# Kernel tuning notes

Hardware: AMD Instinct MI355X
Metric: run time of the kernel (lower is better)

Reference implementation:

```python
import jax, jax.numpy as jnp
import numpy as np

D_MODEL = 1024
N_HEADS = 16
B, T = 16, 512


def setup_inputs() -> dict:
    key = jax.random.key(0)
    ks = jax.random.split(key, 5)
    s = 0.02
    return {
        "x": jax.random.normal(ks[0], (B, T, D_MODEL), dtype=jnp.float32),
        "w_qkv": jax.random.normal(ks[1], (D_MODEL, 3 * D_MODEL), dtype=jnp.float32) * s,
        "b_qkv": jax.random.normal(ks[2], (3 * D_MODEL,), dtype=jnp.float32) * s,
        "w_o": jax.random.normal(ks[3], (D_MODEL, D_MODEL), dtype=jnp.float32) * s,
        "b_o": jax.random.normal(ks[4], (D_MODEL,), dtype=jnp.float32) * s,
    }


def reference(x, w_qkv, b_qkv, w_o, b_o):
    Bx, Tx, C = x.shape
    H = N_HEADS
    hd = C // H
    qkv = x @ w_qkv + b_qkv                      # [B,T,3C]
    qkv = qkv.reshape(Bx, Tx, 3, H, hd).transpose(2, 0, 3, 1, 4)  # [3,B,H,T,hd]
    q, k, v = qkv[0], qkv[1], qkv[2]
    # NOTE: original scales by sqrt(C) = sqrt(d_model), not sqrt(head_dim)
    att = jnp.einsum("bhqd,bhkd->bhqk", q, k) / jnp.sqrt(jnp.float32(C))
    causal = jnp.tril(jnp.ones((Tx, Tx), dtype=bool))
    att = jnp.where(causal, att, -jnp.inf)
    att = jax.nn.softmax(att, axis=-1)
    y = jnp.einsum("bhqk,bhkd->bhqd", att, v)    # [B,H,T,hd]
    y = y.transpose(0, 2, 1, 3).reshape(Bx, Tx, C)
    return y @ w_o + b_o
```

## Files before the change

### kernel.cpp

```cpp
#include <hip/hip_runtime.h>
#include <cstddef>


#define B_  16
#define T_  512
#define C_  1024
#define H_  16
#define HD_ 64

typedef __bf16 bf16x8 __attribute__((ext_vector_type(8)));
typedef float  f32x4  __attribute__((ext_vector_type(4)));

__device__ __forceinline__ void gload16(const void* g, void* lds_dst) {
  __builtin_amdgcn_global_load_lds(
      (const __attribute__((address_space(1))) unsigned int*)g,
      (__attribute__((address_space(3))) unsigned int*)lds_dst, 16, 0, 0);
}

__global__ void cvt_kernel(const float* __restrict__ in, __bf16* __restrict__ out, int n) {
  int i = (blockIdx.x * 256 + threadIdx.x) * 8;
  if (i >= n) return;
  float4 f0 = *(const float4*)&in[i];
  float4 f1 = *(const float4*)&in[i + 4];
  bf16x8 o;
  o[0] = (__bf16)f0.x; o[1] = (__bf16)f0.y; o[2] = (__bf16)f0.z; o[3] = (__bf16)f0.w;
  o[4] = (__bf16)f1.x; o[5] = (__bf16)f1.y; o[6] = (__bf16)f1.z; o[7] = (__bf16)f1.w;
  *(bf16x8*)&out[i] = o;
}

__global__ void tconv_kernel(const float* __restrict__ w, __bf16* __restrict__ wt,
                             int K, int N) {
  __shared__ float tile[32][33];
  int tx = threadIdx.x, ty = threadIdx.y;
  int n0 = blockIdx.x * 32, k0 = blockIdx.y * 32;
  #pragma unroll
  for (int i = 0; i < 4; ++i) {
    int r = ty + i * 8;
    tile[r][tx] = w[(size_t)(k0 + r) * N + n0 + tx];
  }
  __syncthreads();
  #pragma unroll
  for (int i = 0; i < 4; ++i) {
    int r = ty + i * 8;
    wt[(size_t)(n0 + r) * K + k0 + tx] = (__bf16)tile[tx][r];
  }
}

__global__ __launch_bounds__(256) void gemmsq_kernel(
    const __bf16* __restrict__ A, const __bf16* __restrict__ BT,
    const float* __restrict__ bias, int K, int NBn,
    __bf16* __restrict__ oq, __bf16* __restrict__ okk, __bf16* __restrict__ ovt)
{
  __shared__ __attribute__((aligned(16))) char lds[32768];
  const int tid = threadIdx.x, lane = tid & 63, wid = tid >> 6;
  const int wm = wid >> 1, wn = wid & 1;
  const int lr = lane & 15, lg = lane >> 4;

  const int cpx = gridDim.x >> 3;
  const int id = (blockIdx.x & 7) * cpx + (blockIdx.x >> 3);
  const int m0 = (id / NBn) * 128, n0 = (id % NBn) * 128;

  const int r8  = wid * 8 + (lane >> 3);
  const int csw = ((lane & 7) ^ (lane >> 3)) * 8;

  auto stage = [&](const __bf16* g, char* dst) {
    #pragma unroll
    for (int i = 0; i < 4; ++i)
      gload16(g + (size_t)(i * 32 + r8) * K + csw, dst + i * 4096 + wid * 1024);
  };
  auto rd = [&](bf16x8* d, const char* buf, int woff) {
    #pragma unroll
    for (int f = 0; f < 4; ++f) {
      const char* rp = buf + (woff + f * 16 + lr) * 128;
      #pragma unroll
      for (int ks = 0; ks < 2; ++ks)
        d[f * 2 + ks] = *(const bf16x8*)(rp + (((ks << 2) + lg) ^ (lr & 7)) * 16);
    }
  };

  f32x4 acc[4][4] = {};
  const int nt = K >> 6;
  const __bf16* gA = A  + (size_t)m0 * K;
  const __bf16* gB = BT + (size_t)n0 * K;
  char* const Ab = lds;
  char* const Bb = lds + 16384;

  stage(gA, Ab);
  stage(gB, Bb);
  asm volatile("s_waitcnt vmcnt(0)\ns_barrier" ::: "memory");

  bf16x8 a[8], b[8];
  for (int t = 0; t < nt; ++t) {
    rd(a, Ab, wm * 64);
    rd(b, Bb, wn * 64);
    asm volatile("s_waitcnt lgkmcnt(0)\ns_barrier" ::: "memory");
    if (t + 1 < nt) {
      stage(gA + (size_t)(t + 1) * 64, Ab);
      stage(gB + (size_t)(t + 1) * 64, Bb);
    }
    __builtin_amdgcn_s_setprio(1);
    #pragma unroll
    for (int mf = 0; mf < 4; ++mf)
      #pragma unroll
      for (int nf = 0; nf < 4; ++nf)
        #pragma unroll
        for (int ks = 0; ks < 2; ++ks)
          acc[mf][nf] = __builtin_amdgcn_mfma_f32_16x16x32_bf16(
              a[mf * 2 + ks], b[nf * 2 + ks], acc[mf][nf], 0, 0, 0);
    __builtin_amdgcn_s_setprio(0);
    asm volatile("s_waitcnt vmcnt(0)\ns_barrier" ::: "memory");
  }

  #pragma unroll
  for (int nf = 0; nf < 4; ++nf) {
    int n = n0 + wn * 64 + nf * 16 + lr;
    float bv = bias[n];
    int which = n >> 10;
    int h = (n >> 6) & 15, d = n & 63;
    if (which == 2) {
      #pragma unroll
      for (int mf = 0; mf < 4; ++mf) {
        int m = m0 + wm * 64 + mf * 16 + lg * 4;
        int bb = m >> 9, t0 = m & 511;
        ushort4 pk;
        __bf16 e0 = (__bf16)(acc[mf][nf][0] + bv);
        __bf16 e1 = (__bf16)(acc[mf][nf][1] + bv);
        __bf16 e2 = (__bf16)(acc[mf][nf][2] + bv);
        __bf16 e3 = (__bf16)(acc[mf][nf][3] + bv);
        pk.x = *(unsigned short*)&e0; pk.y = *(unsigned short*)&e1;
        pk.z = *(unsigned short*)&e2; pk.w = *(unsigned short*)&e3;
        *(ushort4*)&ovt[(size_t)((bb * H_ + h) * HD_ + d) * T_ + t0] = pk;
      }
    } else {
      __bf16* dst = (which == 0) ? oq : okk;
      #pragma unroll
      for (int mf = 0; mf < 4; ++mf)
        #pragma unroll
        for (int j = 0; j < 4; ++j) {
          int m = m0 + wm * 64 + mf * 16 + lg * 4 + j;
          int bb = m >> 9, tt = m & 511;
          dst[(size_t)((bb * H_ + h) * T_ + tt) * HD_ + d] =
              (__bf16)(acc[mf][nf][j] + bv);
        }
    }
  }
}

__global__ __launch_bounds__(256) void gemmsq_o_kernel(
    const __bf16* __restrict__ A, const __bf16* __restrict__ BT,
    const float* __restrict__ bias, int K, int NBn, int N,
    float* __restrict__ out32)
{
  __shared__ __attribute__((aligned(16))) char lds[32768];
  const int tid = threadIdx.x, lane = tid & 63, wid = tid >> 6;
  const int wm = wid >> 1, wn = wid & 1;
  const int lr = lane & 15, lg = lane >> 4;

  const int cpx = gridDim.x >> 3;
  const int id = (blockIdx.x & 7) * cpx + (blockIdx.x >> 3);
  const int m0 = (id / NBn) * 128, n0 = (id % NBn) * 128;

  const int r8  = wid * 8 + (lane >> 3);
  const int csw = ((lane & 7) ^ (lane >> 3)) * 8;

  auto stage = [&](const __bf16* g, char* dst) {
    #pragma unroll
    for (int i = 0; i < 4; ++i)
      gload16(g + (size_t)(i * 32 + r8) * K + csw, dst + i * 4096 + wid * 1024);
  };
  auto rd = [&](bf16x8* d, const char* buf, int woff) {
    #pragma unroll
    for (int f = 0; f < 4; ++f) {
      const char* rp = buf + (woff + f * 16 + lr) * 128;
      #pragma unroll
      for (int ks = 0; ks < 2; ++ks)
        d[f * 2 + ks] = *(const bf16x8*)(rp + (((ks << 2) + lg) ^ (lr & 7)) * 16);
    }
  };

  f32x4 acc[4][4] = {};
  const int nt = K >> 6;
  const __bf16* gA = A  + (size_t)m0 * K;
  const __bf16* gB = BT + (size_t)n0 * K;
  char* const Ab = lds;
  char* const Bb = lds + 16384;

  stage(gA, Ab);
  stage(gB, Bb);
  asm volatile("s_waitcnt vmcnt(0)\ns_barrier" ::: "memory");

  bf16x8 a[8], b[8];
  for (int t = 0; t < nt; ++t) {
    rd(a, Ab, wm * 64);
    rd(b, Bb, wn * 64);
    asm volatile("s_waitcnt lgkmcnt(0)\ns_barrier" ::: "memory");
    if (t + 1 < nt) {
      stage(gA + (size_t)(t + 1) * 64, Ab);
      stage(gB + (size_t)(t + 1) * 64, Bb);
    }
    __builtin_amdgcn_s_setprio(1);
    #pragma unroll
    for (int mf = 0; mf < 4; ++mf)
      #pragma unroll
      for (int nf = 0; nf < 4; ++nf)
        #pragma unroll
        for (int ks = 0; ks < 2; ++ks)
          acc[mf][nf] = __builtin_amdgcn_mfma_f32_16x16x32_bf16(
              a[mf * 2 + ks], b[nf * 2 + ks], acc[mf][nf], 0, 0, 0);
    __builtin_amdgcn_s_setprio(0);
    asm volatile("s_waitcnt vmcnt(0)\ns_barrier" ::: "memory");
  }

  #pragma unroll
  for (int nf = 0; nf < 4; ++nf) {
    int n = n0 + wn * 64 + nf * 16 + lr;
    float bv = bias[n];
    #pragma unroll
    for (int mf = 0; mf < 4; ++mf)
      #pragma unroll
      for (int j = 0; j < 4; ++j) {
        int m = m0 + wm * 64 + mf * 16 + lg * 4 + j;
        out32[(size_t)m * N + n] = acc[mf][nf][j] + bv;
      }
  }
}

__global__ __launch_bounds__(256, 2) void attn_kernel(
    const __bf16* __restrict__ qb, const __bf16* __restrict__ kb,
    const __bf16* __restrict__ vtb, __bf16* __restrict__ y)
{
  __shared__ __attribute__((aligned(16))) __bf16 Ks[64][72];
  __shared__ __attribute__((aligned(16))) __bf16 Vt[64][72];
  __shared__ __attribute__((aligned(16))) __bf16 Ps[4][16][72];

  const int tid = threadIdx.x, lane = tid & 63, w = tid >> 6;
  const int lr = lane & 15, lg = lane >> 4;
  const int bh = blockIdx.x, qt = blockIdx.y;
  const size_t base = (size_t)bh * T_ * HD_;
  const int q0 = qt * 64 + w * 16;
  const float SCALE = 0.03125f;
  const float L2E = 1.44269504088896f;

  const int r_  = tid >> 3;
  const int c8_ = (tid & 7) * 8;

  bf16x8 qf[2];
  #pragma unroll
  for (int s = 0; s < 2; ++s)
    qf[s] = *(const bf16x8*)&qb[base + (size_t)(q0 + lr) * HD_ + s * 32 + lg * 8];

  f32x4 acc[4] = {};
  float mrun[4] = { -__builtin_inff(), -__builtin_inff(),
                    -__builtin_inff(), -__builtin_inff() };
  float lrun[4] = { 0.f, 0.f, 0.f, 0.f };

  bf16x8 kk[2], vv[2], kk2[2], vv2[2];
  #pragma unroll
  for (int p = 0; p < 2; ++p) {
    int rr = p * 32 + r_;
    kk[p] = *(const bf16x8*)&kb[base + (size_t)rr * HD_ + c8_];
    vv[p] = *(const bf16x8*)&vtb[base + (size_t)rr * T_ + c8_];
  }

  for (int c = 0; c <= qt; ++c) {
    #pragma unroll
    for (int p = 0; p < 2; ++p) {
      int rr = p * 32 + r_;
      *(bf16x8*)&Ks[rr][c8_] = kk[p];
      *(bf16x8*)&Vt[rr][c8_] = vv[p];
    }
    __syncthreads();

    if (c < qt) {
      #pragma unroll
      for (int p = 0; p < 2; ++p) {
        int rr = p * 32 + r_;
        kk2[p] = *(const bf16x8*)&kb[base + (size_t)(c + 1) * 64 * HD_ + (size_t)rr * HD_ + c8_];
        vv2[p] = *(const bf16x8*)&vtb[base + (size_t)rr * T_ + (c + 1) * 64 + c8_];
      }
    }

    f32x4 sc[4] = {};
    #pragma unroll
    for (int s = 0; s < 2; ++s) {
      #pragma unroll
      for (int cc = 0; cc < 4; ++cc) {
        bf16x8 kf = *(const bf16x8*)&Ks[cc * 16 + lr][s * 32 + lg * 8];
        sc[cc] = __builtin_amdgcn_mfma_f32_16x16x32_bf16(qf[s], kf, sc[cc], 0, 0, 0);
      }
    }

    #pragma unroll
    for (int cc = 0; cc < 4; ++cc)
      #pragma unroll
      for (int j = 0; j < 4; ++j) {
        float v = sc[cc][j] * SCALE;
        if (c == qt) {
          int kv = c * 64 + cc * 16 + lr;
          int qr = q0 + lg * 4 + j;
          if (kv > qr) v = -__builtin_inff();
        }
        sc[cc][j] = v;
      }

    float mx[4];
    #pragma unroll
    for (int j = 0; j < 4; ++j)
      mx[j] = fmaxf(fmaxf(sc[0][j], sc[1][j]), fmaxf(sc[2][j], sc[3][j]));
    #pragma unroll
    for (int msk = 1; msk <= 8; msk <<= 1)
      #pragma unroll
      for (int j = 0; j < 4; ++j)
        mx[j] = fmaxf(mx[j], __shfl_xor(mx[j], msk, 64));
    float corr[4];
    #pragma unroll
    for (int j = 0; j < 4; ++j) {
      float nm = fmaxf(mrun[j], mx[j]);
      corr[j] = exp2f((mrun[j] - nm) * L2E);
      mrun[j] = nm;
    }
    #pragma unroll
    for (int cc = 0; cc < 4; ++cc)
      #pragma unroll
      for (int j = 0; j < 4; ++j)
        sc[cc][j] = exp2f((sc[cc][j] - mrun[j]) * L2E);
    float rs[4];
    #pragma unroll
    for (int j = 0; j < 4; ++j)
      rs[j] = sc[0][j] + sc[1][j] + sc[2][j] + sc[3][j];
    #pragma unroll
    for (int msk = 1; msk <= 8; msk <<= 1)
      #pragma unroll
      for (int j = 0; j < 4; ++j)
        rs[j] += __shfl_xor(rs[j], msk, 64);
    #pragma unroll
    for (int j = 0; j < 4; ++j)
      lrun[j] = lrun[j] * corr[j] + rs[j];
    #pragma unroll
    for (int dd = 0; dd < 4; ++dd)
      #pragma unroll
      for (int j = 0; j < 4; ++j)
        acc[dd][j] *= corr[j];

    #pragma unroll
    for (int cc = 0; cc < 4; ++cc)
      #pragma unroll
      for (int j = 0; j < 4; ++j)
        Ps[w][lg * 4 + j][cc * 16 + lr] = (__bf16)sc[cc][j];

    #pragma unroll
    for (int s = 0; s < 2; ++s) {
      bf16x8 pa = *(const bf16x8*)&Ps[w][lr][s * 32 + lg * 8];
      #pragma unroll
      for (int dd = 0; dd < 4; ++dd) {
        bf16x8 vf = *(const bf16x8*)&Vt[dd * 16 + lr][s * 32 + lg * 8];
        acc[dd] = __builtin_amdgcn_mfma_f32_16x16x32_bf16(pa, vf, acc[dd], 0, 0, 0);
      }
    }
    __syncthreads();
    #pragma unroll
    for (int p = 0; p < 2; ++p) { kk[p] = kk2[p]; vv[p] = vv2[p]; }
  }

  const int b = bh >> 4, h = bh & 15;
  #pragma unroll
  for (int dd = 0; dd < 4; ++dd)
    #pragma unroll
    for (int j = 0; j < 4; ++j) {
      int t = q0 + lg * 4 + j;
      int d = dd * 16 + lr;
      y[((size_t)(b * T_ + t)) * C_ + h * HD_ + d] = (__bf16)(acc[dd][j] / lrun[j]);
    }
}

extern "C" void kernel_launch(void* const* d_in, const int* in_sizes, int n_in,
                              void* d_out, int out_size, void* d_ws, size_t ws_size,
                              hipStream_t stream) {
  const float* x    = (const float*)d_in[0];
  const float* wqkv = (const float*)d_in[1];
  const float* bqkv = (const float*)d_in[2];
  const float* wo   = (const float*)d_in[3];
  const float* bo   = (const float*)d_in[4];
  float* out = (float*)d_out;

  char* ws = (char*)d_ws;
  const size_t MB = 1u << 20;
  __bf16* xb    = (__bf16*)(ws);
  __bf16* wqt   = (__bf16*)(ws + 16 * MB);
  __bf16* wot   = (__bf16*)(ws + 22 * MB);
  __bf16* qbuf  = (__bf16*)(ws + 24 * MB);
  __bf16* kbuf  = (__bf16*)(ws + 40 * MB);
  __bf16* vtbuf = (__bf16*)(ws + 56 * MB);
  __bf16* ybuf  = (__bf16*)(ws + 72 * MB);

  const int NX = B_ * T_ * C_;
  cvt_kernel<<<NX / (256 * 8), 256, 0, stream>>>(x, xb, NX);
  tconv_kernel<<<dim3(3 * C_ / 32, C_ / 32), dim3(32, 8), 0, stream>>>(wqkv, wqt, C_, 3 * C_);
  tconv_kernel<<<dim3(C_ / 32, C_ / 32), dim3(32, 8), 0, stream>>>(wo, wot, C_, C_);

  gemmsq_kernel<<<1536, 256, 0, stream>>>(
      xb, wqt, bqkv, C_, 24, qbuf, kbuf, vtbuf);

  attn_kernel<<<dim3(B_ * H_, T_ / 64), 256, 0, stream>>>(qbuf, kbuf, vtbuf, ybuf);

  gemmsq_o_kernel<<<512, 256, 0, stream>>>(
      ybuf, wot, bo, C_, 8, C_, out);
}
```

Baseline: 139.8 us.

## Restructure attention to 32x32 MFMA with transposed scores and register-resident P

Rewrites the attention kernel so each block covers 128 queries with one 32-query tile per wave, computing S^T with 32x32x16 bf16 MFMA so each lane owns a single query row. The P tile is packed to bf16 and exchanged across lane halves with shuffles instead of going through LDS, which removes the Ps buffer and most cross-lane reductions. K/V LDS tiles are double-buffered, so the trailing barrier is dropped, and waves skip key chunks past their causal limit. Outputs are written as packed 4-element stores. The cost is half as many blocks, more registers per thread, and uneven per-wave work inside a block.

```diff
diff --git a/kernel.cpp b/kernel.cpp
--- a/kernel.cpp
+++ b/kernel.cpp
@@ -10,11 +10,19 @@
 
 typedef __bf16 bf16x8 __attribute__((ext_vector_type(8)));
 typedef float  f32x4  __attribute__((ext_vector_type(4)));
+typedef float  f32x16 __attribute__((ext_vector_type(16)));
 
 __device__ __forceinline__ void gload16(const void* g, void* lds_dst) {
   __builtin_amdgcn_global_load_lds(
       (const __attribute__((address_space(1))) unsigned int*)g,
       (__attribute__((address_space(3))) unsigned int*)lds_dst, 16, 0, 0);
+}
+
+__device__ __forceinline__ unsigned pack2(float a, float b) {
+  __bf16 x = (__bf16)a, y = (__bf16)b;
+  unsigned short ux = __builtin_bit_cast(unsigned short, x);
+  unsigned short uy = __builtin_bit_cast(unsigned short, y);
+  return (unsigned)ux | ((unsigned)uy << 16);
 }
 
 __global__ void cvt_kernel(const float* __restrict__ in, __bf16* __restrict__ out, int n) {
@@ -225,34 +233,34 @@
   }
 }
 
-__global__ __launch_bounds__(256, 2) void attn_kernel(
+__global__ __launch_bounds__(256) void attn_kernel(
     const __bf16* __restrict__ qb, const __bf16* __restrict__ kb,
     const __bf16* __restrict__ vtb, __bf16* __restrict__ y)
 {
-  __shared__ __attribute__((aligned(16))) __bf16 Ks[64][72];
-  __shared__ __attribute__((aligned(16))) __bf16 Vt[64][72];
-  __shared__ __attribute__((aligned(16))) __bf16 Ps[4][16][72];
+  __shared__ __attribute__((aligned(16))) __bf16 Ks[2][64][72];
+  __shared__ __attribute__((aligned(16))) __bf16 Vt[2][64][72];
 
   const int tid = threadIdx.x, lane = tid & 63, w = tid >> 6;
-  const int lr = lane & 15, lg = lane >> 4;
+  const int ql = lane & 31, hi = lane >> 5;
   const int bh = blockIdx.x, qt = blockIdx.y;
   const size_t base = (size_t)bh * T_ * HD_;
-  const int q0 = qt * 64 + w * 16;
+  const int b = bh >> 4, h = bh & 15;
+  const int q0w = qt * 128 + w * 32;
+  const int cl_w = q0w >> 6;
+  const int nc = 2 * qt + 2;
   const float SCALE = 0.03125f;
   const float L2E = 1.44269504088896f;
 
   const int r_  = tid >> 3;
   const int c8_ = (tid & 7) * 8;
 
-  bf16x8 qf[2];
-  #pragma unroll
-  for (int s = 0; s < 2; ++s)
-    qf[s] = *(const bf16x8*)&qb[base + (size_t)(q0 + lr) * HD_ + s * 32 + lg * 8];
-
-  f32x4 acc[4] = {};
-  float mrun[4] = { -__builtin_inff(), -__builtin_inff(),
-                    -__builtin_inff(), -__builtin_inff() };
-  float lrun[4] = { 0.f, 0.f, 0.f, 0.f };
+  bf16x8 qf[4];
+  #pragma unroll
+  for (int s = 0; s < 4; ++s)
+    qf[s] = *(const bf16x8*)&qb[base + (size_t)(q0w + ql) * HD_ + s * 16 + hi * 8];
+
+  f32x16 acc[2] = {};
+  float mrun = -__builtin_inff(), lrun = 0.f;
 
   bf16x8 kk[2], vv[2], kk2[2], vv2[2];
   #pragma unroll
@@ -262,114 +270,120 @@
     vv[p] = *(const bf16x8*)&vtb[base + (size_t)rr * T_ + c8_];
   }
 
-  for (int c = 0; c <= qt; ++c) {
+  for (int c = 0; c < nc; ++c) {
+    const int cb = c & 1;
     #pragma unroll
     for (int p = 0; p < 2; ++p) {
       int rr = p * 32 + r_;
-      *(bf16x8*)&Ks[rr][c8_] = kk[p];
-      *(bf16x8*)&Vt[rr][c8_] = vv[p];
+      *(bf16x8*)&Ks[cb][rr][c8_] = kk[p];
+      *(bf16x8*)&Vt[cb][rr][c8_] = vv[p];
     }
     __syncthreads();
 
-    if (c < qt) {
+    if (c + 1 < nc) {
       #pragma unroll
       for (int p = 0; p < 2; ++p) {
         int rr = p * 32 + r_;
-        kk2[p] = *(const bf16x8*)&kb[base + (size_t)(c + 1) * 64 * HD_ + (size_t)rr * HD_ + c8_];
+        kk2[p] = *(const bf16x8*)&kb[base + (size_t)((c + 1) * 64 + rr) * HD_ + c8_];
         vv2[p] = *(const bf16x8*)&vtb[base + (size_t)rr * T_ + (c + 1) * 64 + c8_];
       }
     }
 
-    f32x4 sc[4] = {};
-    #pragma unroll
-    for (int s = 0; s < 2; ++s) {
-      #pragma unroll
-      for (int cc = 0; cc < 4; ++cc) {
-        bf16x8 kf = *(const bf16x8*)&Ks[cc * 16 + lr][s * 32 + lg * 8];
-        sc[cc] = __builtin_amdgcn_mfma_f32_16x16x32_bf16(qf[s], kf, sc[cc], 0, 0, 0);
+    if (c <= cl_w) {
+      f32x16 sc[2] = {};
+      #pragma unroll
+      for (int ka = 0; ka < 2; ++ka)
+        #pragma unroll
+        for (int s = 0; s < 4; ++s) {
+          bf16x8 kf = *(const bf16x8*)&Ks[cb][ka * 32 + ql][s * 16 + hi * 8];
+          sc[ka] = __builtin_amdgcn_mfma_f32_32x32x16_bf16(kf, qf[s], sc[ka], 0, 0, 0);
+        }
+
+      const int qg = q0w + ql;
+      #pragma unroll
+      for (int ka = 0; ka < 2; ++ka)
+        #pragma unroll
+        for (int r = 0; r < 16; ++r) {
+          float v = sc[ka][r] * SCALE;
+          if (c == cl_w) {
+            int kvg = c * 64 + ka * 32 + (r & 3) + 8 * (r >> 2) + 4 * hi;
+            if (kvg > qg) v = -__builtin_inff();
+          }
+          sc[ka][r] = v;
+        }
+
+      float mx = sc[0][0];
+      #pragma unroll
+      for (int ka = 0; ka < 2; ++ka)
+        #pragma unroll
+        for (int r = 0; r < 16; ++r) mx = fmaxf(mx, sc[ka][r]);
+      mx = fmaxf(mx, __shfl_xor(mx, 32, 64));
+      float nm = fmaxf(mrun, mx);
+      float corr = exp2f((mrun - nm) * L2E);
+      mrun = nm;
+
+      float rs = 0.f;
+      #pragma unroll
+      for (int ka = 0; ka < 2; ++ka)
+        #pragma unroll
+        for (int r = 0; r < 16; ++r) {
+          float p = exp2f((sc[ka][r] - nm) * L2E);
+          sc[ka][r] = p;
+          rs += p;
+        }
+      rs += __shfl_xor(rs, 32, 64);
+      lrun = lrun * corr + rs;
+      #pragma unroll
+      for (int da = 0; da < 2; ++da)
+        #pragma unroll
+        for (int r = 0; r < 16; ++r) acc[da][r] *= corr;
+
+      unsigned pk[2][4][2];
+      #pragma unroll
+      for (int ka = 0; ka < 2; ++ka)
+        #pragma unroll
+        for (int m4 = 0; m4 < 4; ++m4)
+          #pragma unroll
+          for (int jh = 0; jh < 2; ++jh)
+            pk[ka][m4][jh] = pack2(sc[ka][4 * m4 + 2 * jh], sc[ka][4 * m4 + 2 * jh + 1]);
+
+      #pragma unroll
+      for (int sp = 0; sp < 4; ++sp) {
+        const int bb2 = sp & 1, kap = sp >> 1;
+        const int mo = 2 * bb2 + hi;
+        const int mp = 2 * bb2 + (hi ^ 1);
+        unsigned own0 = pk[kap][mo][0], own1 = pk[kap][mo][1];
+        unsigned rcv0 = (unsigned)__shfl_xor((int)pk[kap][mp][0], 32, 64);
+        unsigned rcv1 = (unsigned)__shfl_xor((int)pk[kap][mp][1], 32, 64);
+        uint4 wds;
+        if (hi == 0) { wds.x = own0; wds.y = own1; wds.z = rcv0; wds.w = rcv1; }
+        else         { wds.x = rcv0; wds.y = rcv1; wds.z = own0; wds.w = own1; }
+        bf16x8 pb = __builtin_bit_cast(bf16x8, wds);
+        #pragma unroll
+        for (int da = 0; da < 2; ++da) {
+          bf16x8 vf = *(const bf16x8*)&Vt[cb][da * 32 + ql][sp * 16 + hi * 8];
+          acc[da] = __builtin_amdgcn_mfma_f32_32x32x16_bf16(vf, pb, acc[da], 0, 0, 0);
+        }
       }
     }
 
     #pragma unroll
-    for (int cc = 0; cc < 4; ++cc)
-      #pragma unroll
-      for (int j = 0; j < 4; ++j) {
-        float v = sc[cc][j] * SCALE;
-        if (c == qt) {
-          int kv = c * 64 + cc * 16 + lr;
-          int qr = q0 + lg * 4 + j;
-          if (kv > qr) v = -__builtin_inff();
-        }
-        sc[cc][j] = v;
-      }
-
-    float mx[4];
-    #pragma unroll
-    for (int j = 0; j < 4; ++j)
-      mx[j] = fmaxf(fmaxf(sc[0][j], sc[1][j]), fmaxf(sc[2][j], sc[3][j]));
-    #pragma unroll
-    for (int msk = 1; msk <= 8; msk <<= 1)
-      #pragma unroll
-      for (int j = 0; j < 4; ++j)
-        mx[j] = fmaxf(mx[j], __shfl_xor(mx[j], msk, 64));
-    float corr[4];
-    #pragma unroll
-    for (int j = 0; j < 4; ++j) {
-      float nm = fmaxf(mrun[j], mx[j]);
-      corr[j] = exp2f((mrun[j] - nm) * L2E);
-      mrun[j] = nm;
-    }
-    #pragma unroll
-    for (int cc = 0; cc < 4; ++cc)
-      #pragma unroll
-      for (int j = 0; j < 4; ++j)
-        sc[cc][j] = exp2f((sc[cc][j] - mrun[j]) * L2E);
-    float rs[4];
-    #pragma unroll
-    for (int j = 0; j < 4; ++j)
-      rs[j] = sc[0][j] + sc[1][j] + sc[2][j] + sc[3][j];
-    #pragma unroll
-    for (int msk = 1; msk <= 8; msk <<= 1)
-      #pragma unroll
-      for (int j = 0; j < 4; ++j)
-        rs[j] += __shfl_xor(rs[j], msk, 64);
-    #pragma unroll
-    for (int j = 0; j < 4; ++j)
-      lrun[j] = lrun[j] * corr[j] + rs[j];
-    #pragma unroll
-    for (int dd = 0; dd < 4; ++dd)
-      #pragma unroll
-      for (int j = 0; j < 4; ++j)
-        acc[dd][j] *= corr[j];
-
-    #pragma unroll
-    for (int cc = 0; cc < 4; ++cc)
-      #pragma unroll
-      for (int j = 0; j < 4; ++j)
-        Ps[w][lg * 4 + j][cc * 16 + lr] = (__bf16)sc[cc][j];
-
-    #pragma unroll
-    for (int s = 0; s < 2; ++s) {
-      bf16x8 pa = *(const bf16x8*)&Ps[w][lr][s * 32 + lg * 8];
-      #pragma unroll
-      for (int dd = 0; dd < 4; ++dd) {
-        bf16x8 vf = *(const bf16x8*)&Vt[dd * 16 + lr][s * 32 + lg * 8];
-        acc[dd] = __builtin_amdgcn_mfma_f32_16x16x32_bf16(pa, vf, acc[dd], 0, 0, 0);
-      }
-    }
-    __syncthreads();
-    #pragma unroll
     for (int p = 0; p < 2; ++p) { kk[p] = kk2[p]; vv[p] = vv2[p]; }
   }
 
-  const int b = bh >> 4, h = bh & 15;
-  #pragma unroll
-  for (int dd = 0; dd < 4; ++dd)
-    #pragma unroll
-    for (int j = 0; j < 4; ++j) {
-      int t = q0 + lg * 4 + j;
-      int d = dd * 16 + lr;
-      y[((size_t)(b * T_ + t)) * C_ + h * HD_ + d] = (__bf16)(acc[dd][j] / lrun[j]);
+  float inv = 1.f / lrun;
+  #pragma unroll
+  for (int da = 0; da < 2; ++da)
+    #pragma unroll
+    for (int m4 = 0; m4 < 4; ++m4) {
+      ushort4 pkv;
+      __bf16 e0 = (__bf16)(acc[da][4 * m4 + 0] * inv);
+      __bf16 e1 = (__bf16)(acc[da][4 * m4 + 1] * inv);
+      __bf16 e2 = (__bf16)(acc[da][4 * m4 + 2] * inv);
+      __bf16 e3 = (__bf16)(acc[da][4 * m4 + 3] * inv);
+      pkv.x = *(unsigned short*)&e0; pkv.y = *(unsigned short*)&e1;
+      pkv.z = *(unsigned short*)&e2; pkv.w = *(unsigned short*)&e3;
+      *(ushort4*)&y[(size_t)(b * T_ + q0w + ql) * C_ + h * HD_ + da * 32 + m4 * 8 + hi * 4] = pkv;
     }
 }
 
@@ -401,7 +415,7 @@
   gemmsq_kernel<<<1536, 256, 0, stream>>>(
       xb, wqt, bqkv, C_, 24, qbuf, kbuf, vtbuf);
 
-  attn_kernel<<<dim3(B_ * H_, T_ / 64), 256, 0, stream>>>(qbuf, kbuf, vtbuf, ybuf);
+  attn_kernel<<<dim3(B_ * H_, 4), 256, 0, stream>>>(qbuf, kbuf, vtbuf, ybuf);
 
   gemmsq_o_kernel<<<512, 256, 0, stream>>>(
       ybuf, wot, bo, C_, 8, C_, out);
```

New measurement: 152.6 us. 9.2% more time.

## Load full per-head K/V into LDS once and loop query groups per block

Applied to the files above, without the earlier changes.

The attention kernel now launches one 512-thread block per (batch, head). Each block loads the whole K and transposed V for that head into about 146 KB of dynamic LDS through direct global-to-LDS loads with an XOR swizzle, then each wave processes four 16-row query groups. This removes the repeated K/V reloads and the per-tile barriers of the old 64-query-tile grid. The trade-off is fewer blocks (256), one block per CU because of the large LDS footprint, and causal work that is unevenly balanced across waves.

```diff
diff --git a/kernel.cpp b/kernel.cpp
--- a/kernel.cpp
+++ b/kernel.cpp
@@ -225,152 +225,147 @@
   }
 }
 
-__global__ __launch_bounds__(256, 2) void attn_kernel(
+__global__ __launch_bounds__(512) void attn_kernel(
     const __bf16* __restrict__ qb, const __bf16* __restrict__ kb,
     const __bf16* __restrict__ vtb, __bf16* __restrict__ y)
 {
-  __shared__ __attribute__((aligned(16))) __bf16 Ks[64][72];
-  __shared__ __attribute__((aligned(16))) __bf16 Vt[64][72];
-  __shared__ __attribute__((aligned(16))) __bf16 Ps[4][16][72];
+  extern __shared__ __align__(16) char smem[];
+  char* const Ksb = smem;
+  char* const Vtb = smem + 65536;
+  __bf16* const Ps = (__bf16*)(smem + 131072);
 
   const int tid = threadIdx.x, lane = tid & 63, w = tid >> 6;
   const int lr = lane & 15, lg = lane >> 4;
-  const int bh = blockIdx.x, qt = blockIdx.y;
+  const int bh = blockIdx.x;
   const size_t base = (size_t)bh * T_ * HD_;
-  const int q0 = qt * 64 + w * 16;
+  const int b = bh >> 4, h = bh & 15;
   const float SCALE = 0.03125f;
   const float L2E = 1.44269504088896f;
 
-  const int r_  = tid >> 3;
-  const int c8_ = (tid & 7) * 8;
-
-  bf16x8 qf[2];
-  #pragma unroll
-  for (int s = 0; s < 2; ++s)
-    qf[s] = *(const bf16x8*)&qb[base + (size_t)(q0 + lr) * HD_ + s * 32 + lg * 8];
-
-  f32x4 acc[4] = {};
-  float mrun[4] = { -__builtin_inff(), -__builtin_inff(),
-                    -__builtin_inff(), -__builtin_inff() };
-  float lrun[4] = { 0.f, 0.f, 0.f, 0.f };
-
-  bf16x8 kk[2], vv[2], kk2[2], vv2[2];
-  #pragma unroll
-  for (int p = 0; p < 2; ++p) {
-    int rr = p * 32 + r_;
-    kk[p] = *(const bf16x8*)&kb[base + (size_t)rr * HD_ + c8_];
-    vv[p] = *(const bf16x8*)&vtb[base + (size_t)rr * T_ + c8_];
-  }
-
-  for (int c = 0; c <= qt; ++c) {
-    #pragma unroll
-    for (int p = 0; p < 2; ++p) {
-      int rr = p * 32 + r_;
-      *(bf16x8*)&Ks[rr][c8_] = kk[p];
-      *(bf16x8*)&Vt[rr][c8_] = vv[p];
-    }
-    __syncthreads();
-
-    if (c < qt) {
-      #pragma unroll
-      for (int p = 0; p < 2; ++p) {
-        int rr = p * 32 + r_;
-        kk2[p] = *(const bf16x8*)&kb[base + (size_t)(c + 1) * 64 * HD_ + (size_t)rr * HD_ + c8_];
-        vv2[p] = *(const bf16x8*)&vtb[base + (size_t)rr * T_ + (c + 1) * 64 + c8_];
-      }
-    }
-
-    f32x4 sc[4] = {};
-    #pragma unroll
-    for (int s = 0; s < 2; ++s) {
-      #pragma unroll
-      for (int cc = 0; cc < 4; ++cc) {
-        bf16x8 kf = *(const bf16x8*)&Ks[cc * 16 + lr][s * 32 + lg * 8];
-        sc[cc] = __builtin_amdgcn_mfma_f32_16x16x32_bf16(qf[s], kf, sc[cc], 0, 0, 0);
-      }
-    }
-
-    #pragma unroll
-    for (int cc = 0; cc < 4; ++cc)
+  {
+    const int rk = tid >> 3;
+    const int sk = (tid & 7) ^ (rk & 7);
+    const int rv = tid >> 6;
+    const int sv = (tid & 63) ^ rv;
+    #pragma unroll
+    for (int i = 0; i < 8; ++i) {
+      gload16(kb  + base + (size_t)(i * 64 + rk) * HD_ + sk * 8,
+              Ksb + i * 8192 + w * 1024);
+      gload16(vtb + base + (size_t)(i * 8 + rv) * T_ + sv * 8,
+              Vtb + i * 8192 + w * 1024);
+    }
+  }
+  asm volatile("s_waitcnt vmcnt(0)\ns_barrier" ::: "memory");
+
+  #pragma unroll 1
+  for (int k = 0; k < 4; ++k) {
+    const int G = w + 8 * k;
+    const int q0 = G * 16;
+    const int cG = G >> 2;
+
+    bf16x8 qf[2];
+    #pragma unroll
+    for (int s = 0; s < 2; ++s)
+      qf[s] = *(const bf16x8*)&qb[base + (size_t)(q0 + lr) * HD_ + s * 32 + lg * 8];
+
+    f32x4 acc[4] = {};
+    float mrun[4] = { -__builtin_inff(), -__builtin_inff(),
+                      -__builtin_inff(), -__builtin_inff() };
+    float lrun[4] = { 0.f, 0.f, 0.f, 0.f };
+
+    for (int c = 0; c <= cG; ++c) {
+      f32x4 sc[4] = {};
+      #pragma unroll
+      for (int s = 0; s < 2; ++s) {
+        #pragma unroll
+        for (int cc = 0; cc < 4; ++cc) {
+          const char* kp = Ksb + (size_t)(c * 64 + cc * 16 + lr) * 128
+                               + (((s << 2) + lg) ^ (lr & 7)) * 16;
+          bf16x8 kf = *(const bf16x8*)kp;
+          sc[cc] = __builtin_amdgcn_mfma_f32_16x16x32_bf16(qf[s], kf, sc[cc], 0, 0, 0);
+        }
+      }
+
+      #pragma unroll
+      for (int cc = 0; cc < 4; ++cc)
+        #pragma unroll
+        for (int j = 0; j < 4; ++j) {
+          float v = sc[cc][j] * SCALE;
+          if (c == cG) {
+            int kv = c * 64 + cc * 16 + lr;
+            int qr = q0 + lg * 4 + j;
+            if (kv > qr) v = -__builtin_inff();
+          }
+          sc[cc][j] = v;
+        }
+
+      float mx[4];
+      #pragma unroll
+      for (int j = 0; j < 4; ++j)
+        mx[j] = fmaxf(fmaxf(sc[0][j], sc[1][j]), fmaxf(sc[2][j], sc[3][j]));
+      #pragma unroll
+      for (int msk = 1; msk <= 8; msk <<= 1)
+        #pragma unroll
+        for (int j = 0; j < 4; ++j)
+          mx[j] = fmaxf(mx[j], __shfl_xor(mx[j], msk, 64));
+      float corr[4];
       #pragma unroll
       for (int j = 0; j < 4; ++j) {
-        float v = sc[cc][j] * SCALE;
-        if (c == qt) {
-          int kv = c * 64 + cc * 16 + lr;
-          int qr = q0 + lg * 4 + j;
-          if (kv > qr) v = -__builtin_inff();
+        float nm = fmaxf(mrun[j], mx[j]);
+        corr[j] = exp2f((mrun[j] - nm) * L2E);
+        mrun[j] = nm;
+      }
+      #pragma unroll
+      for (int cc = 0; cc < 4; ++cc)
+        #pragma unroll
+        for (int j = 0; j < 4; ++j)
+          sc[cc][j] = exp2f((sc[cc][j] - mrun[j]) * L2E);
+      float rs[4];
+      #pragma unroll
+      for (int j = 0; j < 4; ++j)
+        rs[j] = sc[0][j] + sc[1][j] + sc[2][j] + sc[3][j];
+      #pragma unroll
+      for (int msk = 1; msk <= 8; msk <<= 1)
+        #pragma unroll
+        for (int j = 0; j < 4; ++j)
+          rs[j] += __shfl_xor(rs[j], msk, 64);
+      #pragma unroll
+      for (int j = 0; j < 4; ++j)
+        lrun[j] = lrun[j] * corr[j] + rs[j];
+      #pragma unroll
+      for (int dd = 0; dd < 4; ++dd)
+        #pragma unroll
+        for (int j = 0; j < 4; ++j)
+          acc[dd][j] *= corr[j];
+
+      #pragma unroll
+      for (int cc = 0; cc < 4; ++cc)
+        #pragma unroll
+        for (int j = 0; j < 4; ++j)
+          Ps[((w * 16) + lg * 4 + j) * 72 + cc * 16 + lr] = (__bf16)sc[cc][j];
+
+      #pragma unroll
+      for (int s = 0; s < 2; ++s) {
+        bf16x8 pa = *(const bf16x8*)&Ps[((w * 16) + lr) * 72 + s * 32 + lg * 8];
+        #pragma unroll
+        for (int dd = 0; dd < 4; ++dd) {
+          const char* vp = Vtb + (size_t)(dd * 16 + lr) * 1024
+                               + (8 * c + (((s << 2) + lg) ^ (lr & 7))) * 16;
+          bf16x8 vf = *(const bf16x8*)vp;
+          acc[dd] = __builtin_amdgcn_mfma_f32_16x16x32_bf16(pa, vf, acc[dd], 0, 0, 0);
         }
-        sc[cc][j] = v;
-      }
-
-    float mx[4];
-    #pragma unroll
-    for (int j = 0; j < 4; ++j)
-      mx[j] = fmaxf(fmaxf(sc[0][j], sc[1][j]), fmaxf(sc[2][j], sc[3][j]));
-    #pragma unroll
-    for (int msk = 1; msk <= 8; msk <<= 1)
-      #pragma unroll
-      for (int j = 0; j < 4; ++j)
-        mx[j] = fmaxf(mx[j], __shfl_xor(mx[j], msk, 64));
-    float corr[4];
-    #pragma unroll
-    for (int j = 0; j < 4; ++j) {
-      float nm = fmaxf(mrun[j], mx[j]);
-      corr[j] = exp2f((mrun[j] - nm) * L2E);
-      mrun[j] = nm;
-    }
-    #pragma unroll
-    for (int cc = 0; cc < 4; ++cc)
-      #pragma unroll
-      for (int j = 0; j < 4; ++j)
-        sc[cc][j] = exp2f((sc[cc][j] - mrun[j]) * L2E);
-    float rs[4];
-    #pragma unroll
-    for (int j = 0; j < 4; ++j)
-      rs[j] = sc[0][j] + sc[1][j] + sc[2][j] + sc[3][j];
-    #pragma unroll
-    for (int msk = 1; msk <= 8; msk <<= 1)
-      #pragma unroll
-      for (int j = 0; j < 4; ++j)
-        rs[j] += __shfl_xor(rs[j], msk, 64);
-    #pragma unroll
-    for (int j = 0; j < 4; ++j)
-      lrun[j] = lrun[j] * corr[j] + rs[j];
+      }
+    }
+
     #pragma unroll
     for (int dd = 0; dd < 4; ++dd)
       #pragma unroll
-      for (int j = 0; j < 4; ++j)
-        acc[dd][j] *= corr[j];
-
-    #pragma unroll
-    for (int cc = 0; cc < 4; ++cc)
-      #pragma unroll
-      for (int j = 0; j < 4; ++j)
-        Ps[w][lg * 4 + j][cc * 16 + lr] = (__bf16)sc[cc][j];
-
-    #pragma unroll
-    for (int s = 0; s < 2; ++s) {
-      bf16x8 pa = *(const bf16x8*)&Ps[w][lr][s * 32 + lg * 8];
-      #pragma unroll
-      for (int dd = 0; dd < 4; ++dd) {
-        bf16x8 vf = *(const bf16x8*)&Vt[dd * 16 + lr][s * 32 + lg * 8];
-        acc[dd] = __builtin_amdgcn_mfma_f32_16x16x32_bf16(pa, vf, acc[dd], 0, 0, 0);
-      }
-    }
-    __syncthreads();
-    #pragma unroll
-    for (int p = 0; p < 2; ++p) { kk[p] = kk2[p]; vv[p] = vv2[p]; }
-  }
-
-  const int b = bh >> 4, h = bh & 15;
-  #pragma unroll
-  for (int dd = 0; dd < 4; ++dd)
-    #pragma unroll
-    for (int j = 0; j < 4; ++j) {
-      int t = q0 + lg * 4 + j;
-      int d = dd * 16 + lr;
-      y[((size_t)(b * T_ + t)) * C_ + h * HD_ + d] = (__bf16)(acc[dd][j] / lrun[j]);
-    }
+      for (int j = 0; j < 4; ++j) {
+        int t = q0 + lg * 4 + j;
+        int d = dd * 16 + lr;
+        y[((size_t)(b * T_ + t)) * C_ + h * HD_ + d] = (__bf16)(acc[dd][j] / lrun[j]);
+      }
+  }
 }
 
 extern "C" void kernel_launch(void* const* d_in, const int* in_sizes, int n_in,
@@ -393,6 +388,9 @@
   __bf16* vtbuf = (__bf16*)(ws + 56 * MB);
   __bf16* ybuf  = (__bf16*)(ws + 72 * MB);
 
+  (void)hipFuncSetAttribute(reinterpret_cast<const void*>(&attn_kernel),
+                            hipFuncAttributeMaxDynamicSharedMemorySize, 149504);
+
   const int NX = B_ * T_ * C_;
   cvt_kernel<<<NX / (256 * 8), 256, 0, stream>>>(x, xb, NX);
   tconv_kernel<<<dim3(3 * C_ / 32, C_ / 32), dim3(32, 8), 0, stream>>>(wqkv, wqt, C_, 3 * C_);
@@ -401,7 +399,7 @@
   gemmsq_kernel<<<1536, 256, 0, stream>>>(
       xb, wqt, bqkv, C_, 24, qbuf, kbuf, vtbuf);
 
-  attn_kernel<<<dim3(B_ * H_, T_ / 64), 256, 0, stream>>>(qbuf, kbuf, vtbuf, ybuf);
+  attn_kernel<<<256, 512, 149504, stream>>>(qbuf, kbuf, vtbuf, ybuf);
 
   gemmsq_o_kernel<<<512, 256, 0, stream>>>(
       ybuf, wot, bo, C_, 8, C_, out);
```

Result: no change. 142.2 us (+1.8%).
